# Optimization experiments

Measured on AMD Instinct MI355X. Metric: run time of the kernel, lower is better.

The kernel has to match this reference:

```python
import jax, jax.numpy as jnp
import numpy as np

IN_DIM, HIDDEN, CLASSES, NBASIS = 1024, 4096, 1000, 16

def setup_inputs() -> dict:
    key = jax.random.key(0)
    ks = jax.random.split(key, 7)
    x = jax.random.normal(ks[0], (4096, IN_DIM), dtype=jnp.float32)
    # FerroelectricBasis params: per-feature tanh basis (centers, scales) + dense mix
    centers = jax.random.normal(ks[1], (IN_DIM, NBASIS), dtype=jnp.float32)
    scales = jax.random.uniform(ks[2], (IN_DIM, NBASIS), dtype=jnp.float32, minval=0.5, maxval=2.0)
    s = 1.0 / np.sqrt(IN_DIM * NBASIS)
    Wb = jax.random.uniform(ks[3], (IN_DIM * NBASIS, HIDDEN), dtype=jnp.float32, minval=-s, maxval=s)
    bb = jax.random.uniform(ks[4], (HIDDEN,), dtype=jnp.float32, minval=-s, maxval=s)
    sh = 1.0 / np.sqrt(HIDDEN)
    Wh = jax.random.uniform(ks[5], (HIDDEN, CLASSES), dtype=jnp.float32, minval=-sh, maxval=sh)
    bh = jax.random.uniform(ks[6], (CLASSES,), dtype=jnp.float32, minval=-sh, maxval=sh)
    return {"x": x, "centers": centers, "scales": scales, "Wb": Wb, "bb": bb, "Wh": Wh, "bh": bh}

def reference(x, centers, scales, Wb, bb, Wh, bh):
    B = x.shape[0]
    # ferroelectric (hysteresis-like) tanh basis expansion: [B, in_dim, num_basis]
    feats = jnp.tanh((x[:, :, None] - centers[None]) * scales[None])
    feats = feats.reshape(B, -1)                      # [B, in_dim*num_basis]
    h = feats @ Wb + bb                               # [B, hidden]
    phi = jax.nn.sigmoid(h)
    logits = phi @ Wh + bh                            # [B, num_classes]
    return logits
```

## Files before the change

### kernel.cpp

```cpp
#include <hip/hip_runtime.h>
#include <hip/hip_bf16.h>

typedef __bf16 bf16x8_t __attribute__((ext_vector_type(8)));
typedef float f32x4_t __attribute__((ext_vector_type(4)));
typedef int i32x4_t __attribute__((ext_vector_type(4)));
typedef int i32x8_t __attribute__((ext_vector_type(8)));

#define GLDS(gp, lp) __builtin_amdgcn_global_load_lds(                        \
    (const __attribute__((address_space(1))) void*)(gp),                      \
    (__attribute__((address_space(3))) void*)(lp), 16, 0, 0)

__device__ __forceinline__ float fast_tanh(float z) {
  float zc = fminf(10.0f, fmaxf(-10.0f, z));
  float e = __expf(2.0f * zc);
  return 1.0f - 2.0f / (e + 1.0f);
}

__device__ __forceinline__ int pack_fp8x4(float a, float b, float c, float d) {
  int w = __builtin_amdgcn_cvt_pk_fp8_f32(a, b, 0, false);
  w = __builtin_amdgcn_cvt_pk_fp8_f32(c, d, w, true);
  return w;
}

__global__ __launch_bounds__(256) void feats_kernel(
    const float* __restrict__ x, const float* __restrict__ c,
    const float* __restrict__ s, unsigned char* __restrict__ out) {
  int idx = blockIdx.x * 256 + threadIdx.x;
  int d = idx & 1023;
  float xv = x[idx];
  const float4* c4 = (const float4*)(c + d * 16);
  const float4* s4 = (const float4*)(s + d * 16);
  int w[4];
#pragma unroll
  for (int g = 0; g < 4; ++g) {
    float4 cc = c4[g], ss = s4[g];
    float t0 = fast_tanh((xv - cc.x) * ss.x);
    float t1 = fast_tanh((xv - cc.y) * ss.y);
    float t2 = fast_tanh((xv - cc.z) * ss.z);
    float t3 = fast_tanh((xv - cc.w) * ss.w);
    w[g] = pack_fp8x4(t0, t1, t2, t3);
  }
  *(uint4*)(out + (size_t)idx * 16) = make_uint4(w[0], w[1], w[2], w[3]);
}

__global__ __launch_bounds__(256) void transpose_fp8(
    const float* __restrict__ src, unsigned char* __restrict__ dst, int R, int C) {
  __shared__ float tile[64][65];
  const int c0 = blockIdx.x * 64, r0 = blockIdx.y * 64;
  const int t = threadIdx.x;
  const int rr = t >> 4, cc4 = (t & 15) * 4;
#pragma unroll
  for (int p = 0; p < 4; ++p) {
    int row = rr + p * 16;
    float4 v = *(const float4*)(src + (size_t)(r0 + row) * C + c0 + cc4);
    tile[row][cc4 + 0] = v.x;
    tile[row][cc4 + 1] = v.y;
    tile[row][cc4 + 2] = v.z;
    tile[row][cc4 + 3] = v.w;
  }
  __syncthreads();
  const int drow = t >> 2, seg = (t & 3) * 16;
  int w[4];
#pragma unroll
  for (int g = 0; g < 4; ++g) {
    float a = tile[seg + g * 4 + 0][drow] * 128.0f;
    float b = tile[seg + g * 4 + 1][drow] * 128.0f;
    float cc = tile[seg + g * 4 + 2][drow] * 128.0f;
    float d = tile[seg + g * 4 + 3][drow] * 128.0f;
    w[g] = pack_fp8x4(a, b, cc, d);
  }
  *(uint4*)(dst + (size_t)(c0 + drow) * R + r0 + seg) = make_uint4(w[0], w[1], w[2], w[3]);
}

__global__ __launch_bounds__(256) void transpose_cast(
    const float* __restrict__ src, __hip_bfloat16* __restrict__ dst,
    int R, int C, int Cpad) {
  __shared__ float tile[64][65];
  const int c0 = blockIdx.x * 64, r0 = blockIdx.y * 64;
  const int t = threadIdx.x;
  const int rr = t >> 4, cc4 = (t & 15) * 4;
#pragma unroll
  for (int p = 0; p < 4; ++p) {
    int row = rr + p * 16;
    int cbase = c0 + cc4;
    float4 v;
    if (cbase + 3 < C) {
      v = *(const float4*)(src + (size_t)(r0 + row) * C + cbase);
    } else {
      v.x = (cbase + 0 < C) ? src[(size_t)(r0 + row) * C + cbase + 0] : 0.0f;
      v.y = (cbase + 1 < C) ? src[(size_t)(r0 + row) * C + cbase + 1] : 0.0f;
      v.z = (cbase + 2 < C) ? src[(size_t)(r0 + row) * C + cbase + 2] : 0.0f;
      v.w = (cbase + 3 < C) ? src[(size_t)(r0 + row) * C + cbase + 3] : 0.0f;
    }
    tile[row][cc4 + 0] = v.x;
    tile[row][cc4 + 1] = v.y;
    tile[row][cc4 + 2] = v.z;
    tile[row][cc4 + 3] = v.w;
  }
  __syncthreads();
#pragma unroll
  for (int p = 0; p < 2; ++p) {
    int i = t + 256 * p;
    int drow = i >> 3;
    int seg = (i & 7) * 8;
    int dc = c0 + drow;
    alignas(16) __hip_bfloat16 vals[8];
#pragma unroll
    for (int j = 0; j < 8; ++j) vals[j] = __float2bfloat16(tile[seg + j][drow]);
    if (dc < Cpad)
      *(uint4*)(dst + (size_t)dc * R + r0 + seg) = *(const uint4*)vals;
  }
}

__global__ __launch_bounds__(512, 2) void gemm1_mx8(
    const unsigned char* __restrict__ A, const unsigned char* __restrict__ Bt,
    const float* __restrict__ bias, __hip_bfloat16* __restrict__ outb,
    int M, int N, int K) {
  __shared__ unsigned char As[2][256 * 128];
  __shared__ unsigned char Bs[2][256 * 128];
  const int tid = threadIdx.x;
  const int wave = tid >> 6, lane = tid & 63;
  const int wm = (wave >> 2) * 128, wn = (wave & 3) * 64;

  const int bid = blockIdx.x;
  const int swz = (bid & 7) * 32 + (bid >> 3);
  const int gq = swz >> 5, u = swz & 31;
  const int gm0 = ((gq >> 1) * 4 + (u >> 3)) * 256;
  const int gn0 = ((gq & 1) * 8 + (u & 7)) * 256;

  const unsigned char* ga[4];
  const unsigned char* gb[4];
  int ldso[4];
#pragma unroll
  for (int p = 0; p < 4; ++p) {
    int c = p * 512 + tid;
    int row = c >> 3;
    int g = (c & 7) ^ (row & 7);
    ga[p] = A + (size_t)(gm0 + row) * K + g * 16;
    gb[p] = Bt + (size_t)(gn0 + row) * K + g * 16;
    ldso[p] = c * 16;
  }

  f32x4_t acc[8][4] = {};
  const int fr = lane & 15, kh = lane >> 4;

#pragma unroll
  for (int p = 0; p < 4; ++p) {
    GLDS(ga[p], &As[0][ldso[p]]);
    GLDS(gb[p], &Bs[0][ldso[p]]);
  }

  const int NT = K >> 7;
  for (int t = 0; t < NT; ++t) {
    const unsigned char* Ac = As[t & 1];
    const unsigned char* Bc = Bs[t & 1];

    if (t + 1 < NT) {
      unsigned char* An = (unsigned char*)As[(t + 1) & 1];
      unsigned char* Bn = (unsigned char*)Bs[(t + 1) & 1];
      const int k1 = (t + 1) << 7;
#pragma unroll
      for (int p = 0; p < 4; ++p) {
        GLDS(ga[p] + k1, An + ldso[p]);
        GLDS(gb[p] + k1, Bn + ldso[p]);
      }
      asm volatile("s_waitcnt vmcnt(8)" ::: "memory");
    } else {
      asm volatile("s_waitcnt vmcnt(0)" ::: "memory");
    }
    __builtin_amdgcn_s_barrier();
    __builtin_amdgcn_sched_barrier(0);

    i32x8_t b[4];
#pragma unroll
    for (int j = 0; j < 4; ++j) {
      int rb = wn + j * 16 + fr, sb = rb & 7;
      i32x4_t blo = *(const i32x4_t*)(Bc + rb * 128 + (((2 * kh) ^ sb) * 16));
      i32x4_t bhi = *(const i32x4_t*)(Bc + rb * 128 + (((2 * kh + 1) ^ sb) * 16));
      b[j] = __builtin_shufflevector(blo, bhi, 0, 1, 2, 3, 4, 5, 6, 7);
    }

#pragma unroll
    for (int p = 0; p < 4; ++p) {
      i32x8_t a0, a1;
      {
        int ra = wm + (2 * p + 0) * 16 + fr, sa = ra & 7;
        i32x4_t lo = *(const i32x4_t*)(Ac + ra * 128 + (((2 * kh) ^ sa) * 16));
        i32x4_t hi = *(const i32x4_t*)(Ac + ra * 128 + (((2 * kh + 1) ^ sa) * 16));
        a0 = __builtin_shufflevector(lo, hi, 0, 1, 2, 3, 4, 5, 6, 7);
      }
      {
        int ra = wm + (2 * p + 1) * 16 + fr, sa = ra & 7;
        i32x4_t lo = *(const i32x4_t*)(Ac + ra * 128 + (((2 * kh) ^ sa) * 16));
        i32x4_t hi = *(const i32x4_t*)(Ac + ra * 128 + (((2 * kh + 1) ^ sa) * 16));
        a1 = __builtin_shufflevector(lo, hi, 0, 1, 2, 3, 4, 5, 6, 7);
      }
      __builtin_amdgcn_s_barrier();
      __builtin_amdgcn_s_setprio(1);
#pragma unroll
      for (int j = 0; j < 4; ++j) {
        acc[2 * p + 0][j] = __builtin_amdgcn_mfma_scale_f32_16x16x128_f8f6f4(
            a0, b[j], acc[2 * p + 0][j], 0, 0, 0, 0x7F7F7F7F, 0, 0x7F7F7F7F);
        acc[2 * p + 1][j] = __builtin_amdgcn_mfma_scale_f32_16x16x128_f8f6f4(
            a1, b[j], acc[2 * p + 1][j], 0, 0, 0, 0x7F7F7F7F, 0, 0x7F7F7F7F);
      }
      __builtin_amdgcn_s_setprio(0);
    }
    __builtin_amdgcn_s_barrier();
  }

  const int cn = lane & 15, cm = (lane >> 4) * 4;
#pragma unroll
  for (int j = 0; j < 4; ++j) {
    int n = gn0 + wn + j * 16 + cn;
    float bv = bias[n];
#pragma unroll
    for (int i = 0; i < 8; ++i) {
#pragma unroll
      for (int r = 0; r < 4; ++r) {
        int m = gm0 + wm + i * 16 + cm + r;
        float v = acc[i][j][r] * 0.0078125f + bv;
        float phi = 1.0f / (1.0f + __expf(-v));
        outb[(size_t)m * N + n] = __float2bfloat16(phi);
      }
    }
  }
}

__global__ __launch_bounds__(256) void gemm2_full(
    const __hip_bfloat16* __restrict__ A, const __hip_bfloat16* __restrict__ Bt,
    const float* __restrict__ bh, float* __restrict__ out,
    int M, int N, int K) {
  __shared__ __hip_bfloat16 As[2][2][128 * 32];
  __shared__ __hip_bfloat16 Bs[2][2][128 * 32];
  const int tid = threadIdx.x;
  const int wave = tid >> 6, lane = tid & 63;
  const int wm = (wave >> 1) * 64, wn = (wave & 1) * 64;
  const int gm0 = blockIdx.y * 128, gn0 = blockIdx.x * 128;

  const int t1 = tid, t2 = tid + 256;
  const __hip_bfloat16* Ag0 = A + (size_t)(gm0 + (t1 >> 2)) * K + (t1 & 3) * 8;
  const __hip_bfloat16* Ag1 = A + (size_t)(gm0 + (t2 >> 2)) * K + (t2 & 3) * 8;
  const __hip_bfloat16* Bg0 = Bt + (size_t)(gn0 + (t1 >> 2)) * K + (t1 & 3) * 8;
  const __hip_bfloat16* Bg1 = Bt + (size_t)(gn0 + (t2 >> 2)) * K + (t2 & 3) * 8;

  f32x4_t acc[4][4] = {};
  const int fr = lane & 15, fk = (lane >> 4) * 8;

#pragma unroll
  for (int h = 0; h < 2; ++h) {
    GLDS(Ag0 + h * 32, &As[0][h][t1 * 8]);
    GLDS(Ag1 + h * 32, &As[0][h][t2 * 8]);
    GLDS(Bg0 + h * 32, &Bs[0][h][t1 * 8]);
    GLDS(Bg1 + h * 32, &Bs[0][h][t2 * 8]);
  }
  Ag0 += 64; Ag1 += 64; Bg0 += 64; Bg1 += 64;

  const int nk = K >> 6;
  for (int it = 0; it < nk; ++it) {
    const int cur = it & 1;
    if (it + 1 < nk) {
      const int nxt = cur ^ 1;
#pragma unroll
      for (int h = 0; h < 2; ++h) {
        GLDS(Ag0 + h * 32, &As[nxt][h][t1 * 8]);
        GLDS(Ag1 + h * 32, &As[nxt][h][t2 * 8]);
        GLDS(Bg0 + h * 32, &Bs[nxt][h][t1 * 8]);
        GLDS(Bg1 + h * 32, &Bs[nxt][h][t2 * 8]);
      }
      Ag0 += 64; Ag1 += 64; Bg0 += 64; Bg1 += 64;
      asm volatile("s_waitcnt vmcnt(8)" ::: "memory");
    } else {
      asm volatile("s_waitcnt vmcnt(0)" ::: "memory");
    }
    __builtin_amdgcn_s_barrier();
    __builtin_amdgcn_sched_barrier(0);
#pragma unroll
    for (int h = 0; h < 2; ++h) {
      bf16x8_t a[4], b[4];
#pragma unroll
      for (int i = 0; i < 4; ++i) {
        a[i] = *(const bf16x8_t*)(&As[cur][h][(wm + i * 16 + fr) * 32 + fk]);
        b[i] = *(const bf16x8_t*)(&Bs[cur][h][(wn + i * 16 + fr) * 32 + fk]);
      }
#pragma unroll
      for (int i = 0; i < 4; ++i)
#pragma unroll
        for (int j = 0; j < 4; ++j)
          acc[i][j] = __builtin_amdgcn_mfma_f32_16x16x32_bf16(a[i], b[j], acc[i][j], 0, 0, 0);
    }
    __builtin_amdgcn_s_barrier();
  }

  const int cn = lane & 15, cm = (lane >> 4) * 4;
#pragma unroll
  for (int j = 0; j < 4; ++j) {
    int n = gn0 + wn + j * 16 + cn;
    if (n < 1000) {
      float bv = bh[n];
#pragma unroll
      for (int i = 0; i < 4; ++i)
#pragma unroll
        for (int r = 0; r < 4; ++r) {
          int m = gm0 + wm + i * 16 + cm + r;
          out[(size_t)m * 1000 + n] = acc[i][j][r] + bv;
        }
    }
  }
}

extern "C" void kernel_launch(void* const* d_in, const int* in_sizes, int n_in,
                              void* d_out, int out_size, void* d_ws, size_t ws_size,
                              hipStream_t stream) {
  const float* x = (const float*)d_in[0];
  const float* centers = (const float*)d_in[1];
  const float* scales = (const float*)d_in[2];
  const float* Wb = (const float*)d_in[3];
  const float* bb = (const float*)d_in[4];
  const float* Wh = (const float*)d_in[5];
  const float* bh = (const float*)d_in[6];
  float* out = (float*)d_out;

  unsigned char* feats = (unsigned char*)d_ws;
  unsigned char* Wbt = feats + (size_t)4096 * 16384;
  __hip_bfloat16* phi = (__hip_bfloat16*)(Wbt + (size_t)4096 * 16384);
  __hip_bfloat16* Wht = phi + (size_t)4096 * 4096;

  feats_kernel<<<dim3(16384), dim3(256), 0, stream>>>(x, centers, scales, feats);
  transpose_fp8<<<dim3(64, 256), dim3(256), 0, stream>>>(Wb, Wbt, 16384, 4096);
  transpose_cast<<<dim3(16, 64), dim3(256), 0, stream>>>(Wh, Wht, 4096, 1000, 1024);
  gemm1_mx8<<<dim3(256), dim3(512), 0, stream>>>(feats, Wbt, bb, phi, 4096, 4096, 16384);
  gemm2_full<<<dim3(8, 32), dim3(256), 0, stream>>>(phi, Wht, bh, out, 4096, 1024, 4096);
}
```

Before: 873.1 us.

## Interleave tile prefetch with MFMA phases and double-buffer A fragments in GEMMs

In the FP8 hidden-layer GEMM, next-tile global-to-LDS loads are now issued one chunk per MFMA phase instead of all up front. A-fragment LDS reads for the next phase are issued before the current phase's MFMAs, so register loads overlap matrix math. The explicit vmcnt waits are replaced by a __syncthreads at the end of each K iteration, which relies on that barrier's implied waitcnt to make the LDS writes visible. The bf16 output GEMM gets the same barrier change. This exposes the full load latency at each iteration end instead of the partial vmcnt(8) wait, and raises register pressure.

```diff
diff --git a/kernel.cpp b/kernel.cpp
--- a/kernel.cpp
+++ b/kernel.cpp
@@ -149,27 +149,16 @@
     GLDS(ga[p], &As[0][ldso[p]]);
     GLDS(gb[p], &Bs[0][ldso[p]]);
   }
+  __syncthreads();
 
   const int NT = K >> 7;
   for (int t = 0; t < NT; ++t) {
     const unsigned char* Ac = As[t & 1];
     const unsigned char* Bc = Bs[t & 1];
-
-    if (t + 1 < NT) {
-      unsigned char* An = (unsigned char*)As[(t + 1) & 1];
-      unsigned char* Bn = (unsigned char*)Bs[(t + 1) & 1];
-      const int k1 = (t + 1) << 7;
-#pragma unroll
-      for (int p = 0; p < 4; ++p) {
-        GLDS(ga[p] + k1, An + ldso[p]);
-        GLDS(gb[p] + k1, Bn + ldso[p]);
-      }
-      asm volatile("s_waitcnt vmcnt(8)" ::: "memory");
-    } else {
-      asm volatile("s_waitcnt vmcnt(0)" ::: "memory");
-    }
-    __builtin_amdgcn_s_barrier();
-    __builtin_amdgcn_sched_barrier(0);
+    unsigned char* An = (unsigned char*)As[(t + 1) & 1];
+    unsigned char* Bn = (unsigned char*)Bs[(t + 1) & 1];
+    const int k1 = (t + 1) << 7;
+    const bool pre = (t + 1 < NT);
 
     i32x8_t b[4];
 #pragma unroll
@@ -180,22 +169,44 @@
       b[j] = __builtin_shufflevector(blo, bhi, 0, 1, 2, 3, 4, 5, 6, 7);
     }
 
+    i32x8_t a0, a1;
+    {
+      int ra = wm + 0 * 16 + fr, sa = ra & 7;
+      i32x4_t lo = *(const i32x4_t*)(Ac + ra * 128 + (((2 * kh) ^ sa) * 16));
+      i32x4_t hi = *(const i32x4_t*)(Ac + ra * 128 + (((2 * kh + 1) ^ sa) * 16));
+      a0 = __builtin_shufflevector(lo, hi, 0, 1, 2, 3, 4, 5, 6, 7);
+    }
+    {
+      int ra = wm + 1 * 16 + fr, sa = ra & 7;
+      i32x4_t lo = *(const i32x4_t*)(Ac + ra * 128 + (((2 * kh) ^ sa) * 16));
+      i32x4_t hi = *(const i32x4_t*)(Ac + ra * 128 + (((2 * kh + 1) ^ sa) * 16));
+      a1 = __builtin_shufflevector(lo, hi, 0, 1, 2, 3, 4, 5, 6, 7);
+    }
+
 #pragma unroll
     for (int p = 0; p < 4; ++p) {
-      i32x8_t a0, a1;
-      {
-        int ra = wm + (2 * p + 0) * 16 + fr, sa = ra & 7;
-        i32x4_t lo = *(const i32x4_t*)(Ac + ra * 128 + (((2 * kh) ^ sa) * 16));
-        i32x4_t hi = *(const i32x4_t*)(Ac + ra * 128 + (((2 * kh + 1) ^ sa) * 16));
-        a0 = __builtin_shufflevector(lo, hi, 0, 1, 2, 3, 4, 5, 6, 7);
-      }
-      {
-        int ra = wm + (2 * p + 1) * 16 + fr, sa = ra & 7;
-        i32x4_t lo = *(const i32x4_t*)(Ac + ra * 128 + (((2 * kh) ^ sa) * 16));
-        i32x4_t hi = *(const i32x4_t*)(Ac + ra * 128 + (((2 * kh + 1) ^ sa) * 16));
-        a1 = __builtin_shufflevector(lo, hi, 0, 1, 2, 3, 4, 5, 6, 7);
+      if (pre) {
+        GLDS(ga[p] + k1, An + ldso[p]);
+        GLDS(gb[p] + k1, Bn + ldso[p]);
       }
       __builtin_amdgcn_s_barrier();
+
+      i32x8_t na0, na1;
+      if (p < 3) {
+        {
+          int ra = wm + (2 * p + 2) * 16 + fr, sa = ra & 7;
+          i32x4_t lo = *(const i32x4_t*)(Ac + ra * 128 + (((2 * kh) ^ sa) * 16));
+          i32x4_t hi = *(const i32x4_t*)(Ac + ra * 128 + (((2 * kh + 1) ^ sa) * 16));
+          na0 = __builtin_shufflevector(lo, hi, 0, 1, 2, 3, 4, 5, 6, 7);
+        }
+        {
+          int ra = wm + (2 * p + 3) * 16 + fr, sa = ra & 7;
+          i32x4_t lo = *(const i32x4_t*)(Ac + ra * 128 + (((2 * kh) ^ sa) * 16));
+          i32x4_t hi = *(const i32x4_t*)(Ac + ra * 128 + (((2 * kh + 1) ^ sa) * 16));
+          na1 = __builtin_shufflevector(lo, hi, 0, 1, 2, 3, 4, 5, 6, 7);
+        }
+      }
+
       __builtin_amdgcn_s_setprio(1);
 #pragma unroll
       for (int j = 0; j < 4; ++j) {
@@ -205,8 +216,13 @@
             a1, b[j], acc[2 * p + 1][j], 0, 0, 0, 0x7F7F7F7F, 0, 0x7F7F7F7F);
       }
       __builtin_amdgcn_s_setprio(0);
-    }
-    __builtin_amdgcn_s_barrier();
+      if (p < 3) {
+        a0 = na0;
+        a1 = na1;
+        __builtin_amdgcn_s_barrier();
+      }
+    }
+    __syncthreads();
   }
 
   const int cn = lane & 15, cm = (lane >> 4) * 4;
@@ -255,6 +271,7 @@
     GLDS(Bg1 + h * 32, &Bs[0][h][t2 * 8]);
   }
   Ag0 += 64; Ag1 += 64; Bg0 += 64; Bg1 += 64;
+  __syncthreads();
 
   const int nk = K >> 6;
   for (int it = 0; it < nk; ++it) {
@@ -269,12 +286,7 @@
         GLDS(Bg1 + h * 32, &Bs[nxt][h][t2 * 8]);
       }
       Ag0 += 64; Ag1 += 64; Bg0 += 64; Bg1 += 64;
-      asm volatile("s_waitcnt vmcnt(8)" ::: "memory");
-    } else {
-      asm volatile("s_waitcnt vmcnt(0)" ::: "memory");
-    }
-    __builtin_amdgcn_s_barrier();
-    __builtin_amdgcn_sched_barrier(0);
+    }
 #pragma unroll
     for (int h = 0; h < 2; ++h) {
       bf16x8_t a[4], b[4];
@@ -289,7 +301,7 @@
         for (int j = 0; j < 4; ++j)
           acc[i][j] = __builtin_amdgcn_mfma_f32_16x16x32_bf16(a[i], b[j], acc[i][j], 0, 0, 0);
     }
-    __builtin_amdgcn_s_barrier();
+    __syncthreads();
   }
 
   const int cn = lane & 15, cm = (lane >> 4) * 4;
```

Result: faster. 786.1 us (-10.0%).

## Interleave next-tile prefetch with MFMA phases and widen fp8 transpose tiles

Applied to the files above, without the earlier changes.

In the fp8 GEMM, global-to-LDS prefetches for the next K tile are now spread across the first three MFMA sub-phases instead of being issued all at once at the top of the loop. The explicit vmcnt waits are replaced with __syncthreads at the end of each iteration, and the bf16 GEMM gets the same change. The aim is to overlap memory issue with matrix compute and reduce stalls at the start of each iteration. The Wb transpose now handles 128 rows per block and writes two 16-byte stores per thread, which halves the block count and lengthens each contiguous output run. The trade-off is that each iteration now ends with a full vmcnt(0) drain, which may remove some of the overlap the old double-buffer waits allowed.

```diff
diff --git a/kernel.cpp b/kernel.cpp
--- a/kernel.cpp
+++ b/kernel.cpp
@@ -45,31 +45,33 @@
 
 __global__ __launch_bounds__(256) void transpose_fp8(
     const float* __restrict__ src, unsigned char* __restrict__ dst, int R, int C) {
-  __shared__ float tile[64][65];
-  const int c0 = blockIdx.x * 64, r0 = blockIdx.y * 64;
+  __shared__ float tile[128][65];
+  const int c0 = blockIdx.x * 64, r0 = blockIdx.y * 128;
   const int t = threadIdx.x;
-  const int rr = t >> 4, cc4 = (t & 15) * 4;
-#pragma unroll
-  for (int p = 0; p < 4; ++p) {
-    int row = rr + p * 16;
-    float4 v = *(const float4*)(src + (size_t)(r0 + row) * C + c0 + cc4);
-    tile[row][cc4 + 0] = v.x;
-    tile[row][cc4 + 1] = v.y;
-    tile[row][cc4 + 2] = v.z;
-    tile[row][cc4 + 3] = v.w;
+  const int rr = t >> 4, fc = (t & 15) * 4;
+#pragma unroll
+  for (int q = 0; q < 8; ++q) {
+    int row = rr + q * 16;
+    float4 v = *(const float4*)(src + (size_t)(r0 + row) * C + c0 + fc);
+    tile[row][fc + 0] = v.x;
+    tile[row][fc + 1] = v.y;
+    tile[row][fc + 2] = v.z;
+    tile[row][fc + 3] = v.w;
   }
   __syncthreads();
-  const int drow = t >> 2, seg = (t & 3) * 16;
-  int w[4];
-#pragma unroll
-  for (int g = 0; g < 4; ++g) {
-    float a = tile[seg + g * 4 + 0][drow] * 128.0f;
-    float b = tile[seg + g * 4 + 1][drow] * 128.0f;
-    float cc = tile[seg + g * 4 + 2][drow] * 128.0f;
-    float d = tile[seg + g * 4 + 3][drow] * 128.0f;
-    w[g] = pack_fp8x4(a, b, cc, d);
-  }
-  *(uint4*)(dst + (size_t)(c0 + drow) * R + r0 + seg) = make_uint4(w[0], w[1], w[2], w[3]);
+  const int cc = t >> 2, rbase = (t & 3) * 32;
+  int w[8];
+#pragma unroll
+  for (int g = 0; g < 8; ++g) {
+    float a = tile[rbase + g * 4 + 0][cc] * 128.0f;
+    float b = tile[rbase + g * 4 + 1][cc] * 128.0f;
+    float c2 = tile[rbase + g * 4 + 2][cc] * 128.0f;
+    float d = tile[rbase + g * 4 + 3][cc] * 128.0f;
+    w[g] = pack_fp8x4(a, b, c2, d);
+  }
+  unsigned char* dp = dst + (size_t)(c0 + cc) * R + r0 + rbase;
+  *(uint4*)(dp + 0) = make_uint4(w[0], w[1], w[2], w[3]);
+  *(uint4*)(dp + 16) = make_uint4(w[4], w[5], w[6], w[7]);
 }
 
 __global__ __launch_bounds__(256) void transpose_cast(
@@ -149,27 +151,16 @@
     GLDS(ga[p], &As[0][ldso[p]]);
     GLDS(gb[p], &Bs[0][ldso[p]]);
   }
+  __syncthreads();
 
   const int NT = K >> 7;
   for (int t = 0; t < NT; ++t) {
     const unsigned char* Ac = As[t & 1];
     const unsigned char* Bc = Bs[t & 1];
-
-    if (t + 1 < NT) {
-      unsigned char* An = (unsigned char*)As[(t + 1) & 1];
-      unsigned char* Bn = (unsigned char*)Bs[(t + 1) & 1];
-      const int k1 = (t + 1) << 7;
-#pragma unroll
-      for (int p = 0; p < 4; ++p) {
-        GLDS(ga[p] + k1, An + ldso[p]);
-        GLDS(gb[p] + k1, Bn + ldso[p]);
-      }
-      asm volatile("s_waitcnt vmcnt(8)" ::: "memory");
-    } else {
-      asm volatile("s_waitcnt vmcnt(0)" ::: "memory");
-    }
-    __builtin_amdgcn_s_barrier();
-    __builtin_amdgcn_sched_barrier(0);
+    unsigned char* An = (unsigned char*)As[(t + 1) & 1];
+    unsigned char* Bn = (unsigned char*)Bs[(t + 1) & 1];
+    const int k1 = (t + 1) << 7;
+    const bool pre = (t + 1 < NT);
 
     i32x8_t b[4];
 #pragma unroll
@@ -182,6 +173,20 @@
 
 #pragma unroll
     for (int p = 0; p < 4; ++p) {
+      if (pre) {
+        if (p == 0) {
+          GLDS(ga[0] + k1, An + ldso[0]);
+          GLDS(gb[0] + k1, Bn + ldso[0]);
+          GLDS(ga[2] + k1, An + ldso[2]);
+        } else if (p == 1) {
+          GLDS(gb[2] + k1, Bn + ldso[2]);
+          GLDS(ga[1] + k1, An + ldso[1]);
+          GLDS(gb[1] + k1, Bn + ldso[1]);
+        } else if (p == 2) {
+          GLDS(ga[3] + k1, An + ldso[3]);
+          GLDS(gb[3] + k1, Bn + ldso[3]);
+        }
+      }
       i32x8_t a0, a1;
       {
         int ra = wm + (2 * p + 0) * 16 + fr, sa = ra & 7;
@@ -205,8 +210,9 @@
             a1, b[j], acc[2 * p + 1][j], 0, 0, 0, 0x7F7F7F7F, 0, 0x7F7F7F7F);
       }
       __builtin_amdgcn_s_setprio(0);
-    }
-    __builtin_amdgcn_s_barrier();
+      if (p < 3) __builtin_amdgcn_s_barrier();
+    }
+    __syncthreads();
   }
 
   const int cn = lane & 15, cm = (lane >> 4) * 4;
@@ -255,6 +261,7 @@
     GLDS(Bg1 + h * 32, &Bs[0][h][t2 * 8]);
   }
   Ag0 += 64; Ag1 += 64; Bg0 += 64; Bg1 += 64;
+  __syncthreads();
 
   const int nk = K >> 6;
   for (int it = 0; it < nk; ++it) {
@@ -269,12 +276,7 @@
         GLDS(Bg1 + h * 32, &Bs[nxt][h][t2 * 8]);
       }
       Ag0 += 64; Ag1 += 64; Bg0 += 64; Bg1 += 64;
-      asm volatile("s_waitcnt vmcnt(8)" ::: "memory");
-    } else {
-      asm volatile("s_waitcnt vmcnt(0)" ::: "memory");
-    }
-    __builtin_amdgcn_s_barrier();
-    __builtin_amdgcn_sched_barrier(0);
+    }
 #pragma unroll
     for (int h = 0; h < 2; ++h) {
       bf16x8_t a[4], b[4];
@@ -289,7 +291,7 @@
         for (int j = 0; j < 4; ++j)
           acc[i][j] = __builtin_amdgcn_mfma_f32_16x16x32_bf16(a[i], b[j], acc[i][j], 0, 0, 0);
     }
-    __builtin_amdgcn_s_barrier();
+    __syncthreads();
   }
 
   const int cn = lane & 15, cm = (lane >> 4) * 4;
@@ -327,7 +329,7 @@
   __hip_bfloat16* Wht = phi + (size_t)4096 * 4096;
 
   feats_kernel<<<dim3(16384), dim3(256), 0, stream>>>(x, centers, scales, feats);
-  transpose_fp8<<<dim3(64, 256), dim3(256), 0, stream>>>(Wb, Wbt, 16384, 4096);
+  transpose_fp8<<<dim3(64, 128), dim3(256), 0, stream>>>(Wb, Wbt, 16384, 4096);
   transpose_cast<<<dim3(16, 64), dim3(256), 0, stream>>>(Wh, Wht, 4096, 1000, 1024);
   gemm1_mx8<<<dim3(256), dim3(512), 0, stream>>>(feats, Wbt, bb, phi, 4096, 4096, 16384);
   gemm2_full<<<dim3(8, 32), dim3(256), 0, stream>>>(phi, Wht, bh, out, 4096, 1024, 4096);
```

New measurement: 766.0 us. -12.3%, faster.
